# Kernel optimization log

Hardware: AMD Instinct MI355X
Metric: run time of the kernel (lower is better)

The kernel has to match this reference:

```python
import jax, jax.numpy as jnp
import numpy as np
from jax import lax

B, IMG = 2, 512
FMC, HID, A, NC = 1024, 512, 9, 21
RED, POOL, TOP, IOU_THR = 16, 7, 20, 0.3
NEG = -1e30
# 3 scales x 3 aspect ratios (w, h)
ANCHOR_WH = np.array([[s * np.sqrt(r), s / np.sqrt(r)] for s in (64.0, 128.0, 256.0) for r in (0.5, 1.0, 2.0)], dtype=np.float32)


def conv(x, w, b, stride, pad):
    y = lax.conv_general_dilated(x, w, (stride, stride), pad, dimension_numbers=('NCHW', 'OIHW', 'NCHW'))
    return y + b[None, :, None, None]


def make_anchors(H, W, stride):
    cy = (jnp.arange(H, dtype=jnp.float32) + 0.5) * stride
    cx = (jnp.arange(W, dtype=jnp.float32) + 0.5) * stride
    cyg, cxg = jnp.meshgrid(cy, cx, indexing='ij')  # [H,W]
    wh = jnp.asarray(ANCHOR_WH)  # [A,2]
    w2 = wh[None, None, :, 0] / 2
    h2 = wh[None, None, :, 1] / 2
    cxg = cxg[:, :, None]
    cyg = cyg[:, :, None]
    boxes = jnp.stack([cxg - w2, cyg - h2, cxg + w2, cyg + h2], axis=-1)  # [H,W,A,4]
    return boxes.reshape(-1, 4)


def box_iou(b, boxes):
    # b [4], boxes [N,4], (x1,y1,x2,y2)
    ix1 = jnp.maximum(b[0], boxes[:, 0])
    iy1 = jnp.maximum(b[1], boxes[:, 1])
    ix2 = jnp.minimum(b[2], boxes[:, 2])
    iy2 = jnp.minimum(b[3], boxes[:, 3])
    inter = jnp.maximum(ix2 - ix1, 0.0) * jnp.maximum(iy2 - iy1, 0.0)
    ab = jnp.maximum(b[2] - b[0], 0.0) * jnp.maximum(b[3] - b[1], 0.0)
    ar = jnp.maximum(boxes[:, 2] - boxes[:, 0], 0.0) * jnp.maximum(boxes[:, 3] - boxes[:, 1], 0.0)
    return inter / (ab + ar - inter + 1e-8)


def nms_one(boxes, scores):
    # greedy NMS, fixed TOP selections
    n = scores.shape[0]
    idxs = jnp.arange(n)

    def step(s, _):
        i = jnp.argmax(s)
        b, sc = boxes[i], s[i]
        s = jnp.where((box_iou(b, boxes) > IOU_THR) | (idxs == i), NEG, s)
        return s, (b, sc)

    _, (bs, ss) = lax.scan(step, scores, None, length=TOP)
    return bs, ss  # [TOP,4], [TOP]


def roi_align_one(fm_b, boxes):
    # fm_b [C,H,W], boxes [R,4] in image coords -> [R,C,POOL,POOL]
    C, H, W = fm_b.shape
    b = boxes / RED
    t = (jnp.arange(POOL, dtype=jnp.float32) + 0.5) / POOL
    xs = b[:, 0:1] + jnp.maximum(b[:, 2] - b[:, 0], 0.0)[:, None] * t[None]  # [R,P]
    ys = b[:, 1:2] + jnp.maximum(b[:, 3] - b[:, 1], 0.0)[:, None] * t[None]
    x = jnp.clip(xs[:, None, :], 0.0, W - 1.0) * jnp.ones((1, POOL, 1), jnp.float32)  # [R,P,P]
    y = jnp.clip(ys[:, :, None], 0.0, H - 1.0) * jnp.ones((1, 1, POOL), jnp.float32)
    x0f, y0f = jnp.floor(x), jnp.floor(y)
    x0, y0 = x0f.astype(jnp.int32), y0f.astype(jnp.int32)
    x1 = jnp.minimum(x0 + 1, W - 1)
    y1 = jnp.minimum(y0 + 1, H - 1)
    lx, ly = x - x0f, y - y0f
    v00 = fm_b[:, y0, x0]
    v01 = fm_b[:, y0, x1]
    v10 = fm_b[:, y1, x0]
    v11 = fm_b[:, y1, x1]  # [C,R,P,P]
    out = v00 * (1 - ly) * (1 - lx) + v01 * (1 - ly) * lx + v10 * ly * (1 - lx) + v11 * ly * lx
    return out.transpose(1, 0, 2, 3)


def setup_inputs() -> dict:
    key = jax.random.key(0)
    ks = jax.random.split(key, 16)
    s = 0.02
    return {
        'img': jax.random.normal(ks[0], (B, 3, IMG, IMG), jnp.float32),
        'img_id': jnp.arange(B, dtype=jnp.int32),
        'cnn_w': jax.random.normal(ks[1], (FMC, 3, RED, RED), jnp.float32) * s,
        'cnn_b': jnp.zeros((FMC,), jnp.float32),
        'rpn_w': jax.random.normal(ks[2], (HID, FMC, 3, 3), jnp.float32) * s,
        'rpn_b': jnp.zeros((HID,), jnp.float32),
        'rpn_reg_w': jax.random.normal(ks[3], (A * 4, HID, 1, 1), jnp.float32) * s,
        'rpn_reg_b': jnp.zeros((A * 4,), jnp.float32),
        'rpn_cls_w': jax.random.normal(ks[4], (A, HID, 1, 1), jnp.float32) * s,
        'rpn_cls_b': jnp.zeros((A,), jnp.float32),
        'fc_w': jax.random.normal(ks[5], (FMC * POOL * POOL, 1024), jnp.float32) * 0.005,
        'fc_b': jnp.zeros((1024,), jnp.float32),
        'reg_w': jax.random.normal(ks[6], (1024, 4), jnp.float32) * s,
        'reg_b': jnp.zeros((4,), jnp.float32),
        'cls_w': jax.random.normal(ks[7], (1024, NC), jnp.float32) * s,
        'cls_b': jnp.zeros((NC,), jnp.float32),
    }


def reference(img, img_id, cnn_w, cnn_b, rpn_w, rpn_b, rpn_reg_w, rpn_reg_b, rpn_cls_w, rpn_cls_b, fc_w, fc_b, reg_w, reg_b, cls_w, cls_b):
    fm = jax.nn.relu(conv(img, cnn_w, cnn_b, RED, 'VALID'))  # [B,1024,32,32]
    Bn, C, H, W = fm.shape
    # sliding-window(3x3, stride 1) + per-slice RPN == 3x3 SAME conv + 1x1 heads
    h = jax.nn.relu(conv(fm, rpn_w, rpn_b, 1, 'SAME'))
    rpn_reg = conv(h, rpn_reg_w, rpn_reg_b, 1, 'SAME').transpose(0, 2, 3, 1).reshape(Bn, -1, 4)  # (h,w,a) order
    rpn_cls = conv(h, rpn_cls_w, rpn_cls_b, 1, 'SAME').transpose(0, 2, 3, 1).reshape(Bn, -1)
    anchors = make_anchors(H, W, RED)  # [H*W*A,4]
    nms_reg, nms_cls = jax.vmap(nms_one)(rpn_reg + anchors[None], rpn_cls)  # [B,TOP,4],[B,TOP]
    pooled = jax.vmap(roi_align_one)(fm[img_id], nms_reg)  # [B,TOP,C,P,P]
    flat = pooled.reshape(Bn * TOP, -1)
    hf = jax.nn.relu(flat @ fc_w + fc_b)
    rcnn_reg = (hf @ reg_w + reg_b).reshape(Bn, -1, 4)
    rcnn_cls = (hf @ cls_w + cls_b).reshape(Bn, TOP, -1)
    return rpn_reg, rpn_cls, nms_reg, nms_cls, rcnn_reg, rcnn_cls, anchors
```

## Files before the change

kernel.cpp:

```cpp
#include <hip/hip_runtime.h>
#include <math.h>


#define NEGV (-1e30f)

typedef unsigned short u16;
typedef float v4f __attribute__((ext_vector_type(4)));
typedef short short8 __attribute__((ext_vector_type(8)));

#define O_RPN_REG 0
#define O_RPN_CLS 73728
#define O_NMS_REG 92160
#define O_NMS_CLS 92320
#define O_RCNN_REG 92360
#define O_RCNN_CLS 92520
#define O_ANCH 93360

#define W_FM   0u
#define W_ZERO 2097152u
#define W_PROP 3145728u
#define W_SCR  3219456u
#define W_FLAT 3237888u
#define W_HF   5244928u
#define W_A1H  5285888u
#define W_A1L  6072320u
#define W_B1H  6858752u
#define W_B1L  7251968u
#define W_FMH  7645184u
#define W_FML  8693760u
#define W_B2H  9742336u
#define W_B2L  12101632u
#define W_PART 14460928u

static __device__ __forceinline__ float relu_(float v) { return fmaxf(v, 0.0f); }

static __device__ __forceinline__ void gload16(const void* g, void* l) {
    __builtin_amdgcn_global_load_lds(
        (const __attribute__((address_space(1))) unsigned int*)g,
        (__attribute__((address_space(3))) unsigned int*)l, 16, 0, 0);
}

static __device__ __forceinline__ u16 bf16_rtne(float x) {
    unsigned int u = __float_as_uint(x);
    unsigned int r = u + 0x7fffu + ((u >> 16) & 1u);
    return (u16)(r >> 16);
}
static __device__ __forceinline__ void split2(float x, u16& h, u16& l) {
    h = bf16_rtne(x);
    const float hf = __uint_as_float(((unsigned int)h) << 16);
    l = bf16_rtne(x - hf);
}
static __device__ __forceinline__ void split8_store(const float* v, u16* dsth, u16* dstl) {
    uint4 H, Lo;
    u16 h0, l0, h1, l1;
    split2(v[0], h0, l0); split2(v[1], h1, l1);
    H.x = (unsigned)h0 | ((unsigned)h1 << 16); Lo.x = (unsigned)l0 | ((unsigned)l1 << 16);
    split2(v[2], h0, l0); split2(v[3], h1, l1);
    H.y = (unsigned)h0 | ((unsigned)h1 << 16); Lo.y = (unsigned)l0 | ((unsigned)l1 << 16);
    split2(v[4], h0, l0); split2(v[5], h1, l1);
    H.z = (unsigned)h0 | ((unsigned)h1 << 16); Lo.z = (unsigned)l0 | ((unsigned)l1 << 16);
    split2(v[6], h0, l0); split2(v[7], h1, l1);
    H.w = (unsigned)h0 | ((unsigned)h1 << 16); Lo.w = (unsigned)l0 | ((unsigned)l1 << 16);
    *(uint4*)dsth = H; *(uint4*)dstl = Lo;
}

static __device__ __forceinline__ void anchor_wh(int a, float& w2, float& h2) {
    double s = (a < 3) ? 64.0 : (a < 6) ? 128.0 : 256.0;
    int rm = a - (a / 3) * 3;
    double r = (rm == 0) ? 0.5 : (rm == 1) ? 1.0 : 2.0;
    double sq = sqrt(r);
    w2 = (float)(s * sq) * 0.5f;
    h2 = (float)(s / sq) * 0.5f;
}

__global__ __launch_bounds__(256) void k_prep_all(
        const float* __restrict__ img, u16* __restrict__ a1h, u16* __restrict__ a1l,
        float* __restrict__ zbuf,
        const float* __restrict__ cnnw, u16* __restrict__ b1h, u16* __restrict__ b1l,
        const float* __restrict__ rpnw, u16* __restrict__ b2h, u16* __restrict__ b2l) {
    __shared__ __align__(16) u16 sh[9216];
    __shared__ __align__(16) u16 sl[9216];
    const int bx = blockIdx.x, tid = threadIdx.x;
    if (bx < 1536) {
        if (bx == 0 && tid < 64) zbuf[tid] = 0.0f;
        const int idx = bx * 256 + tid;
        const int m = idx / 192, kq = (idx - m * 192) * 4;
        const int b = m >> 10, i = (m >> 5) & 31, j = m & 31;
        const int c = kq >> 8, rem = kq & 255, y = rem >> 4, x = rem & 15;
        const float4 v = *(const float4*)(img + ((size_t)((b * 3 + c) * 512 + i * 16 + y)) * 512 + j * 16 + x);
        ushort4 H, Lo;
        split2(v.x, H.x, Lo.x); split2(v.y, H.y, Lo.y);
        split2(v.z, H.z, Lo.z); split2(v.w, H.w, Lo.w);
        *(ushort4*)(a1h + (size_t)idx * 4) = H;
        *(ushort4*)(a1l + (size_t)idx * 4) = Lo;
    } else if (bx < 2304) {
        const int idx = (bx - 1536) * 256 + tid;
        const float4 v = *(const float4*)(cnnw + (size_t)idx * 4);
        ushort4 H, Lo;
        split2(v.x, H.x, Lo.x); split2(v.y, H.y, Lo.y);
        split2(v.z, H.z, Lo.z); split2(v.w, H.w, Lo.w);
        *(ushort4*)(b1h + (size_t)idx * 4) = H;
        *(ushort4*)(b1l + (size_t)idx * 4) = Lo;
    } else {
        const int oc = bx - 2304;
        const float* p = rpnw + (size_t)oc * 9216;
        for (int i = tid * 4; i < 9216; i += 1024) {
            const float4 v = *(const float4*)(p + i);
            ushort4 H, Lo;
            split2(v.x, H.x, Lo.x); split2(v.y, H.y, Lo.y);
            split2(v.z, H.z, Lo.z); split2(v.w, H.w, Lo.w);
            *(ushort4*)(sh + i) = H;
            *(ushort4*)(sl + i) = Lo;
        }
        __syncthreads();
        const int ic4 = tid * 4;
#pragma unroll
        for (int d = 0; d < 9; ++d) {
            ushort4 H, Lo;
            H.x = sh[(ic4 + 0) * 9 + d]; Lo.x = sl[(ic4 + 0) * 9 + d];
            H.y = sh[(ic4 + 1) * 9 + d]; Lo.y = sl[(ic4 + 1) * 9 + d];
            H.z = sh[(ic4 + 2) * 9 + d]; Lo.z = sl[(ic4 + 2) * 9 + d];
            H.w = sh[(ic4 + 3) * 9 + d]; Lo.w = sl[(ic4 + 3) * 9 + d];
            const size_t o = (size_t)oc * 9216 + d * 1024 + ic4;
            *(ushort4*)(b2h + o) = H;
            *(ushort4*)(b2l + o) = Lo;
        }
    }
}

template<int MODE>
__global__ __launch_bounds__(256, 3) void k_gemm(
        const u16* __restrict__ Agh, const u16* __restrict__ Agl,
        const u16* __restrict__ Bgh, const u16* __restrict__ Bgl,
        const float* __restrict__ bias, float* __restrict__ Cout, float* __restrict__ Cout2,
        const int KA, const int KB, const int nchunk, const int ldc, const int do_bias_relu,
        u16* __restrict__ outH, u16* __restrict__ outL, const float* __restrict__ zbuf) {
    __shared__ __align__(16) u16 AsH[2 * 128 * 32];
    __shared__ __align__(16) u16 AsL[2 * 128 * 32];
    __shared__ __align__(16) u16 BsH[2 * 64 * 32];
    __shared__ __align__(16) u16 BsL[2 * 64 * 32];
    const int tid = threadIdx.x;
    const int w = tid >> 6, L = tid & 63;
    const int q = L >> 4, lr = L & 15;
    const int wm = w >> 1, wn = w & 1;
    const int m0 = blockIdx.x * 128, n0 = blockIdx.y * 64;
    const int zbase = blockIdx.z * nchunk;
    float* C;
    if (MODE == 1) {
        C = (blockIdx.z < 4) ? (Cout + (size_t)blockIdx.z * (2048u * 512u))
                             : (Cout2 + (size_t)(blockIdx.z - 4) * (2048u * 512u));
    } else {
        C = (blockIdx.z == 0) ? Cout : Cout2;
    }
    const int seg = L & 3, rsub = L >> 2;

    u16* lseg[6];
    int lsz[6];
    const u16* gbase[6];
    int arow_b[6], arow_i[6], arow_j[6];
    int kindv[6];
#pragma unroll
    for (int s = 0; s < 6; ++s) {
        const int idx = w * 6 + s;
        int kind, inst;
        if (idx < 8)       { kind = 0; inst = idx; }
        else if (idx < 16) { kind = 1; inst = idx - 8; }
        else if (idx < 20) { kind = 2; inst = idx - 16; }
        else               { kind = 3; inst = idx - 20; }
        kindv[s] = kind;
        const int r = inst * 16 + rsub;
        u16* lb = (kind == 0) ? AsH : (kind == 1) ? AsL : (kind == 2) ? BsH : BsL;
        lseg[s] = lb + r * 32 + seg * 8;
        lsz[s] = (kind < 2) ? (128 * 32) : (64 * 32);
        arow_b[s] = 0; arow_i[s] = 0; arow_j[s] = 0;
        if (kind >= 2) {
            const u16* gb = (kind == 2) ? Bgh : Bgl;
            gbase[s] = gb + (size_t)(n0 + r) * KB + seg * 8;
        } else if (MODE == 0) {
            const u16* gb = (kind == 0) ? Agh : Agl;
            gbase[s] = gb + (size_t)(m0 + r) * KA + seg * 8;
        } else {
            const int m = m0 + r;
            arow_b[s] = m >> 10; arow_i[s] = (m >> 5) & 31; arow_j[s] = m & 31;
            gbase[s] = (kind == 0) ? Agh : Agl;
        }
    }

    v4f acc[4][2];
#pragma unroll
    for (int t = 0; t < 4; ++t)
#pragma unroll
        for (int u2 = 0; u2 < 2; ++u2) acc[t][u2] = (v4f){0.f, 0.f, 0.f, 0.f};

#define ISSUE(c_, bb_) do { \
    int d_, ic_, kB_; \
    if (MODE == 0) { const int g_ = zbase + (c_); kB_ = g_ * 32; d_ = 0; ic_ = kB_; } \
    else { const int g_ = zbase + (c_); d_ = g_ >> 5; ic_ = (g_ & 31) << 5; kB_ = d_ * 1024 + ic_; } \
    const int di_ = d_ / 3, dj_ = d_ - di_ * 3; \
    _Pragma("unroll") \
    for (int s = 0; s < 6; ++s) { \
        const u16* gsrc_; \
        if (kindv[s] >= 2) gsrc_ = gbase[s] + kB_; \
        else if (MODE == 0) gsrc_ = gbase[s] + ic_; \
        else { \
            const int y_ = arow_i[s] + di_ - 1, x_ = arow_j[s] + dj_ - 1; \
            const bool ok_ = ((unsigned)y_ < 32u) && ((unsigned)x_ < 32u); \
            const int yc_ = ok_ ? y_ : 0, xc_ = ok_ ? x_ : 0; \
            const u16* ga_ = gbase[s] + (size_t)((arow_b[s] * 32 + yc_) * 32 + xc_) * 1024 + ic_ + seg * 8; \
            gsrc_ = ok_ ? ga_ : (const u16*)zbuf; \
        } \
        gload16(gsrc_, lseg[s] + (bb_) * lsz[s]); \
    } \
} while (0)

    int cur = 0;
    ISSUE(0, 0);
    for (int c = 0; c < nchunk; ++c) {
        __syncthreads();
        if (c + 1 < nchunk) ISSUE(c + 1, cur ^ 1);
        const int ao = cur * (128 * 32), bo = cur * (64 * 32);
        short8 ah[4], al[4], bh[2], bl[2];
#pragma unroll
        for (int t = 0; t < 4; ++t) {
            ah[t] = *(const short8*)(AsH + ao + (wm * 64 + t * 16 + lr) * 32 + q * 8);
            al[t] = *(const short8*)(AsL + ao + (wm * 64 + t * 16 + lr) * 32 + q * 8);
        }
#pragma unroll
        for (int u2 = 0; u2 < 2; ++u2) {
            bh[u2] = *(const short8*)(BsH + bo + (wn * 32 + u2 * 16 + lr) * 32 + q * 8);
            bl[u2] = *(const short8*)(BsL + bo + (wn * 32 + u2 * 16 + lr) * 32 + q * 8);
        }
#pragma unroll
        for (int t = 0; t < 4; ++t)
#pragma unroll
            for (int u2 = 0; u2 < 2; ++u2) {
                acc[t][u2] = __builtin_amdgcn_mfma_f32_16x16x32_bf16(ah[t], bh[u2], acc[t][u2], 0, 0, 0);
                acc[t][u2] = __builtin_amdgcn_mfma_f32_16x16x32_bf16(ah[t], bl[u2], acc[t][u2], 0, 0, 0);
                acc[t][u2] = __builtin_amdgcn_mfma_f32_16x16x32_bf16(al[t], bh[u2], acc[t][u2], 0, 0, 0);
            }
        cur ^= 1;
    }
#undef ISSUE

#pragma unroll
    for (int t = 0; t < 4; ++t) {
        const int row = m0 + wm * 64 + t * 16 + q * 4;
#pragma unroll
        for (int u2 = 0; u2 < 2; ++u2) {
            const int col = n0 + wn * 32 + u2 * 16 + lr;
            const float bv = do_bias_relu ? bias[col] : 0.f;
#pragma unroll
            for (int r = 0; r < 4; ++r) {
                float vv = acc[t][u2][r];
                if (do_bias_relu) vv = relu_(vv + bv);
                C[(size_t)(row + r) * ldc + col] = vv;
                if (MODE == 0 && outH != nullptr) {
                    u16 hh, ll; split2(vv, hh, ll);
                    outH[(size_t)(row + r) * 1024 + col] = hh;
                    outL[(size_t)(row + r) * 1024 + col] = ll;
                }
            }
        }
    }
}

__global__ void k_c1_reduce(const float* __restrict__ p1, const float* __restrict__ cb,
                            float* __restrict__ fm, u16* __restrict__ fmh, u16* __restrict__ fml) {
    const size_t o = ((size_t)blockIdx.x * 256 + threadIdx.x) * 4;
    float4 a = *(const float4*)(fm + o);
    const float4 b4 = *(const float4*)(p1 + o);
    const float4 bb = *(const float4*)(cb + (o & 1023));
    a.x = relu_(a.x + b4.x + bb.x);
    a.y = relu_(a.y + b4.y + bb.y);
    a.z = relu_(a.z + b4.z + bb.z);
    a.w = relu_(a.w + b4.w + bb.w);
    *(float4*)(fm + o) = a;
    ushort4 H, Lo;
    split2(a.x, H.x, Lo.x); split2(a.y, H.y, Lo.y);
    split2(a.z, H.z, Lo.z); split2(a.w, H.w, Lo.w);
    *(ushort4*)(fmh + o) = H;
    *(ushort4*)(fml + o) = Lo;
}

__global__ __launch_bounds__(256) void k_rpn_heads2(const float* __restrict__ partA,
        const float* __restrict__ partB,
        const float* __restrict__ rpnb,
        const float* __restrict__ regw, const float* __restrict__ regb,
        const float* __restrict__ clsw, const float* __restrict__ clsb,
        float* __restrict__ out, float* __restrict__ prop, float* __restrict__ scr) {
    __shared__ __align__(16) float hrow[8][512];
    const int tid = threadIdx.x;
    const int m0 = blockIdx.x * 8;
#pragma unroll
    for (int i = 0; i < 4; ++i) {
        const int f = i * 256 + tid;
        const int r = f >> 7, c4 = (f & 127) * 4;
        const size_t ro = (size_t)(m0 + r) * 512 + c4;
        const float4 a0 = *(const float4*)(partA + ro);
        const float4 a1 = *(const float4*)(partA + 1048576u + ro);
        const float4 a2 = *(const float4*)(partA + 2097152u + ro);
        const float4 a3 = *(const float4*)(partA + 3145728u + ro);
        const float4 a4 = *(const float4*)(partB + ro);
        const float4 a5 = *(const float4*)(partB + 1048576u + ro);
        const float4 bb = *(const float4*)(rpnb + c4);
        float4 o;
        o.x = relu_(a0.x + a1.x + a2.x + a3.x + a4.x + a5.x + bb.x);
        o.y = relu_(a0.y + a1.y + a2.y + a3.y + a4.y + a5.y + bb.y);
        o.z = relu_(a0.z + a1.z + a2.z + a3.z + a4.z + a5.z + bb.z);
        o.w = relu_(a0.w + a1.w + a2.w + a3.w + a4.w + a5.w + bb.w);
        *(float4*)&hrow[r][c4] = o;
    }
    __syncthreads();
    const int w = tid >> 6, lane = tid & 63;
#pragma unroll
    for (int rr = 0; rr < 2; ++rr) {
        const int lrow = w * 2 + rr;
        const int m = m0 + lrow;
        const int b = m >> 10, qd = m & 1023, ii = qd >> 5, jj = qd & 31;
        const float cx = ((float)jj + 0.5f) * 16.f, cy = ((float)ii + 0.5f) * 16.f;
        if (lane < 45) {
            const int isreg = (lane < 36);
            const float* wp = isreg ? (regw + (size_t)lane * 512) : (clsw + (size_t)(lane - 36) * 512);
            float acc2 = isreg ? regb[lane] : clsb[lane - 36];
            const float* hr = hrow[lrow];
            for (int k = 0; k < 512; k += 4) {
                const float4 wv = *(const float4*)(wp + k);
                acc2 += hr[k + 0] * wv.x; acc2 += hr[k + 1] * wv.y;
                acc2 += hr[k + 2] * wv.z; acc2 += hr[k + 3] * wv.w;
            }
            if (isreg) {
                out[O_RPN_REG + (size_t)b * 36864 + qd * 36 + lane] = acc2;
                const int a = lane >> 2, cc = lane & 3;
                float w2, h2; anchor_wh(a, w2, h2);
                const float av = (cc == 0) ? cx - w2 : (cc == 1) ? cy - h2 : (cc == 2) ? cx + w2 : cy + h2;
                prop[(size_t)b * 36864 + qd * 36 + lane] = acc2 + av;
            } else {
                const int n = lane - 36;
                out[O_RPN_CLS + (size_t)b * 9216 + qd * 9 + n] = acc2;
                scr[(size_t)b * 9216 + qd * 9 + n] = acc2;
            }
        } else if (b == 0 && lane < 54) {
            const int a = lane - 45;
            float w2, h2; anchor_wh(a, w2, h2);
            const float4 av4 = make_float4(cx - w2, cy - h2, cx + w2, cy + h2);
            *(float4*)(out + O_ANCH + (size_t)(qd * 9 + a) * 4) = av4;
        }
    }
}

__global__ __launch_bounds__(512) void k_nms3(const float* __restrict__ prop,
        const float* __restrict__ scr, float* __restrict__ out) {
    __shared__ float wv_[2][8];
    __shared__ int wi_[2][8];
    const int b = blockIdx.x, tid = threadIdx.x;
    const int lane = tid & 63, wid = tid >> 6;
    const float* P = prop + (size_t)b * 36864;
    float4 bx[18]; float sv[18];
#pragma unroll
    for (int k = 0; k < 18; ++k) {
        const int i = tid * 18 + k;
        bx[k] = *(const float4*)(P + (size_t)i * 4);
        sv[k] = scr[b * 9216 + i];
    }
    for (int t = 0; t < 20; ++t) {
        float bv = -3.4e38f; int bi = 0;
#pragma unroll
        for (int k = 0; k < 18; ++k)
            if (sv[k] > bv) { bv = sv[k]; bi = tid * 18 + k; }
#pragma unroll
        for (int off = 1; off < 64; off <<= 1) {
            const float ov = __shfl_xor(bv, off);
            const int oi = __shfl_xor(bi, off);
            if (ov > bv || (ov == bv && oi < bi)) { bv = ov; bi = oi; }
        }
        if (lane == 0) { wv_[t & 1][wid] = bv; wi_[t & 1][wid] = bi; }
        __syncthreads();
        float rb = wv_[t & 1][0]; int sel = wi_[t & 1][0];
#pragma unroll
        for (int j = 1; j < 8; ++j) {
            const float v2 = wv_[t & 1][j]; const int i2 = wi_[t & 1][j];
            if (v2 > rb || (v2 == rb && i2 < sel)) { rb = v2; sel = i2; }
        }
        const float4 bb = *(const float4*)(P + (size_t)sel * 4);
        if (tid == 0) {
            *(float4*)(out + O_NMS_REG + (size_t)(b * 20 + t) * 4) = bb;
            out[O_NMS_CLS + b * 20 + t] = rb;
        }
        const float ab2 = fmaxf(bb.z - bb.x, 0.f) * fmaxf(bb.w - bb.y, 0.f);
#pragma unroll
        for (int k = 0; k < 18; ++k) {
            const float ix1 = fmaxf(bb.x, bx[k].x), iy1 = fmaxf(bb.y, bx[k].y);
            const float ix2 = fminf(bb.z, bx[k].z), iy2 = fminf(bb.w, bx[k].w);
            const float inter = fmaxf(ix2 - ix1, 0.f) * fmaxf(iy2 - iy1, 0.f);
            const float ar2 = fmaxf(bx[k].z - bx[k].x, 0.f) * fmaxf(bx[k].w - bx[k].y, 0.f);
            const float iou = inter / (ab2 + ar2 - inter + 1e-8f);
            if (iou > 0.3f || (tid * 18 + k) == sel) sv[k] = NEGV;
        }
    }
}

__global__ __launch_bounds__(256) void k_roi(const float* __restrict__ fm,
        const int* __restrict__ img_id, const float* __restrict__ nreg,
        float* __restrict__ flat, const float* __restrict__ fcb, float* __restrict__ hf) {
    __shared__ float tile[12544];
    const int hid = (((blockIdx.z * 20 + blockIdx.y) * 4) + blockIdx.x) * 256 + threadIdx.x;
    hf[hid] = fcb[hid & 1023];
    const int c0 = blockIdx.x * 256;
    const int roi = blockIdx.y, b = blockIdx.z;
    const float* bx = nreg + (size_t)(b * 20 + roi) * 4;
    const float b0 = bx[0] * 0.0625f, b1 = bx[1] * 0.0625f;
    const float b2 = bx[2] * 0.0625f, b3 = bx[3] * 0.0625f;
    const float wd = fmaxf(b2 - b0, 0.f), hg = fmaxf(b3 - b1, 0.f);
    const int bb = img_id[b];
    const float* fmb = fm + (size_t)bb * (32 * 32 * 1024);
    const int c = c0 + threadIdx.x;
    for (int py = 0; py < 7; ++py) {
        const float tyv = ((float)py + 0.5f) / 7.0f;
        const float ycv = fminf(fmaxf(b1 + hg * tyv, 0.f), 31.f);
        const float y0f = floorf(ycv);
        const int y0 = (int)y0f, y1 = min(y0 + 1, 31);
        const float ly = ycv - y0f, omly = 1.f - ly;
        for (int px = 0; px < 7; ++px) {
            const float txv = ((float)px + 0.5f) / 7.0f;
            const float xcv = fminf(fmaxf(b0 + wd * txv, 0.f), 31.f);
            const float x0f = floorf(xcv);
            const int x0 = (int)x0f, x1 = min(x0 + 1, 31);
            const float lx = xcv - x0f, omlx = 1.f - lx;
            const int o00 = ((y0 * 32) + x0) << 10, o01 = ((y0 * 32) + x1) << 10;
            const int o10 = ((y1 * 32) + x0) << 10, o11 = ((y1 * 32) + x1) << 10;
            const float v00 = fmb[o00 + c], v01 = fmb[o01 + c];
            const float v10 = fmb[o10 + c], v11 = fmb[o11 + c];
            tile[threadIdx.x * 49 + py * 7 + px] =
                ((v00 * omly) * omlx) + ((v01 * omly) * lx)
                + ((v10 * ly) * omlx) + ((v11 * ly) * lx);
        }
    }
    __syncthreads();
    const size_t ob = (size_t)(b * 20 + roi) * 50176 + (size_t)c0 * 49;
    for (int i = threadIdx.x * 4; i < 12544; i += 1024)
        *(float4*)(flat + ob + i) = *(const float4*)&tile[i];
}

__global__ __launch_bounds__(256, 2) void k_fc_mfma(const float* __restrict__ flat,
        const float* __restrict__ fcw, float* __restrict__ hf) {
    __shared__ __align__(16) u16 AsH[4 * 48 * 8];
    __shared__ __align__(16) u16 AsL[4 * 48 * 8];
    __shared__ __align__(16) u16 BsH[4 * 128 * 8];
    __shared__ __align__(16) u16 BsL[4 * 128 * 8];
    const int tid = threadIdx.x;
    const int w = tid >> 6, L = tid & 63, q = L >> 4, lr = L & 15;
    const int n0 = blockIdx.x * 128, kb = blockIdx.y * 512;
    if (tid < 32) {
        const int oct = tid >> 3, m = 40 + (tid & 7);
        *(uint4*)(AsH + (oct * 48 + m) * 8) = make_uint4(0, 0, 0, 0);
        *(uint4*)(AsL + (oct * 48 + m) * 8) = make_uint4(0, 0, 0, 0);
    }
    const int am = tid >> 2, aoct = tid & 3;
    const float* abase = flat + (size_t)am * 50176 + kb + aoct * 8;
    const int bcolI = tid & 127, bkh = tid >> 7;
    const float* bcol = fcw + n0 + bcolI;

    v4f acc[3][2];
#pragma unroll
    for (int mt = 0; mt < 3; ++mt)
#pragma unroll
        for (int nt = 0; nt < 2; ++nt) acc[mt][nt] = (v4f){0.f, 0.f, 0.f, 0.f};

    float areg[8];
    float breg[2][8];

#define LOADF(c_) do { \
    if (tid < 160) { \
        const float4 u_ = *(const float4*)(abase + (c_) * 32); \
        const float4 v_ = *(const float4*)(abase + (c_) * 32 + 4); \
        areg[0] = u_.x; areg[1] = u_.y; areg[2] = u_.z; areg[3] = u_.w; \
        areg[4] = v_.x; areg[5] = v_.y; areg[6] = v_.z; areg[7] = v_.w; \
    } \
    _Pragma("unroll") \
    for (int o_ = 0; o_ < 2; ++o_) \
        _Pragma("unroll") \
        for (int j_ = 0; j_ < 8; ++j_) \
            breg[o_][j_] = bcol[(size_t)(kb + (c_) * 32 + bkh * 16 + o_ * 8 + j_) * 1024]; \
} while (0)

    LOADF(0);
    for (int c = 0; c < 16; ++c) {
        __syncthreads();
        if (tid < 160)
            split8_store(areg, AsH + (aoct * 48 + am) * 8, AsL + (aoct * 48 + am) * 8);
#pragma unroll
        for (int o = 0; o < 2; ++o)
            split8_store(breg[o], BsH + ((bkh * 2 + o) * 128 + bcolI) * 8,
                                  BsL + ((bkh * 2 + o) * 128 + bcolI) * 8);
        __syncthreads();
        if (c + 1 < 16) LOADF(c + 1);
        short8 ah[3], al[3], bh2[2], bl2[2];
#pragma unroll
        for (int mt = 0; mt < 3; ++mt) {
            ah[mt] = *(const short8*)(AsH + (q * 48 + mt * 16 + lr) * 8);
            al[mt] = *(const short8*)(AsL + (q * 48 + mt * 16 + lr) * 8);
        }
#pragma unroll
        for (int nt = 0; nt < 2; ++nt) {
            bh2[nt] = *(const short8*)(BsH + (q * 128 + w * 32 + nt * 16 + lr) * 8);
            bl2[nt] = *(const short8*)(BsL + (q * 128 + w * 32 + nt * 16 + lr) * 8);
        }
#pragma unroll
        for (int mt = 0; mt < 3; ++mt)
#pragma unroll
            for (int nt = 0; nt < 2; ++nt) {
                acc[mt][nt] = __builtin_amdgcn_mfma_f32_16x16x32_bf16(ah[mt], bh2[nt], acc[mt][nt], 0, 0, 0);
                acc[mt][nt] = __builtin_amdgcn_mfma_f32_16x16x32_bf16(ah[mt], bl2[nt], acc[mt][nt], 0, 0, 0);
                acc[mt][nt] = __builtin_amdgcn_mfma_f32_16x16x32_bf16(al[mt], bh2[nt], acc[mt][nt], 0, 0, 0);
            }
    }
#undef LOADF

#pragma unroll
    for (int mt = 0; mt < 3; ++mt) {
#pragma unroll
        for (int nt = 0; nt < 2; ++nt) {
#pragma unroll
            for (int r = 0; r < 4; ++r) {
                const int row = mt * 16 + q * 4 + r;
                if (row < 40)
                    atomicAdd(hf + (size_t)row * 1024 + n0 + w * 32 + nt * 16 + lr, acc[mt][nt][r]);
            }
        }
    }
}

__global__ __launch_bounds__(64) void k_heads(const float* __restrict__ hf,
        const float* __restrict__ regw, const float* __restrict__ regb,
        const float* __restrict__ clsw, const float* __restrict__ clsb,
        float* __restrict__ out) {
    __shared__ __align__(16) float hrow[1024];
    const int m = blockIdx.x, tid = threadIdx.x;
    for (int i = tid * 4; i < 1024; i += 256) {
        const float4 v = *(const float4*)(hf + (size_t)m * 1024 + i);
        hrow[i + 0] = relu_(v.x); hrow[i + 1] = relu_(v.y);
        hrow[i + 2] = relu_(v.z); hrow[i + 3] = relu_(v.w);
    }
    __syncthreads();
    if (tid < 25) {
        float acc2 = 0.f;
        if (tid < 4) {
            for (int k = 0; k < 1024; ++k) acc2 += hrow[k] * regw[(size_t)k * 4 + tid];
            out[O_RCNN_REG + m * 4 + tid] = acc2 + regb[tid];
        } else {
            const int n = tid - 4;
            for (int k = 0; k < 1024; ++k) acc2 += hrow[k] * clsw[(size_t)k * 21 + n];
            out[O_RCNN_CLS + m * 21 + n] = acc2 + clsb[n];
        }
    }
}

extern "C" void kernel_launch(void* const* d_in, const int* in_sizes, int n_in,
                              void* d_out, int out_size, void* d_ws, size_t ws_size,
                              hipStream_t stream) {
    (void)in_sizes; (void)n_in; (void)out_size; (void)ws_size;
    const float* img       = (const float*)d_in[0];
    const int*   img_id    = (const int*)  d_in[1];
    const float* cnn_w     = (const float*)d_in[2];
    const float* cnn_b     = (const float*)d_in[3];
    const float* rpn_w     = (const float*)d_in[4];
    const float* rpn_b     = (const float*)d_in[5];
    const float* rpn_reg_w = (const float*)d_in[6];
    const float* rpn_reg_b = (const float*)d_in[7];
    const float* rpn_cls_w = (const float*)d_in[8];
    const float* rpn_cls_b = (const float*)d_in[9];
    const float* fc_w      = (const float*)d_in[10];
    const float* fc_b      = (const float*)d_in[11];
    const float* reg_w     = (const float*)d_in[12];
    const float* reg_b     = (const float*)d_in[13];
    const float* cls_w     = (const float*)d_in[14];
    const float* cls_b     = (const float*)d_in[15];
    float* out = (float*)d_out;
    float* ws  = (float*)d_ws;

    float* fm   = ws + W_FM;
    float* zbuf = ws + W_ZERO;
    float* prop = ws + W_PROP;
    float* scr  = ws + W_SCR;
    float* flat = ws + W_FLAT;
    float* hf   = ws + W_HF;
    u16* a1h = (u16*)(ws + W_A1H);
    u16* a1l = (u16*)(ws + W_A1L);
    u16* b1h = (u16*)(ws + W_B1H);
    u16* b1l = (u16*)(ws + W_B1L);
    u16* fmh = (u16*)(ws + W_FMH);
    u16* fml = (u16*)(ws + W_FML);
    u16* b2h = (u16*)(ws + W_B2H);
    u16* b2l = (u16*)(ws + W_B2L);
    float* partA = ws + W_FLAT;
    float* partB = ws + W_PART;

    k_prep_all<<<2816, 256, 0, stream>>>(img, a1h, a1l, zbuf, cnn_w, b1h, b1l, rpn_w, b2h, b2l);
    k_gemm<0><<<dim3(16, 16, 2), 256, 0, stream>>>(a1h, a1l, b1h, b1l, cnn_b, fm, partB,
                                                   768, 768, 12, 1024, 0, nullptr, nullptr, zbuf);
    k_c1_reduce<<<2048, 256, 0, stream>>>(partB, cnn_b, fm, fmh, fml);
    k_gemm<1><<<dim3(16, 8, 6), 256, 0, stream>>>(fmh, fml, b2h, b2l, nullptr, partA, partB,
                                                  1024, 9216, 48, 512, 0, nullptr, nullptr, zbuf);
    k_rpn_heads2<<<256, 256, 0, stream>>>(partA, partB, rpn_b, rpn_reg_w, rpn_reg_b, rpn_cls_w, rpn_cls_b,
                                          out, prop, scr);
    k_nms3<<<2, 512, 0, stream>>>(prop, scr, out);
    k_roi<<<dim3(4, 20, 2), 256, 0, stream>>>(fm, img_id, out + O_NMS_REG, flat, fc_b, hf);
    k_fc_mfma<<<dim3(8, 98), 256, 0, stream>>>(flat, fc_w, hf);
    k_heads<<<40, 64, 0, stream>>>(hf, reg_w, reg_b, cls_w, cls_b, out);
}
```

Before: 605.4 us.

## Use 128x128 GEMM tiles with atomic split-K accumulation into bias-initialized outputs

The split-bf16 MFMA GEMM tile grows from 128x64 to 128x128, giving each warp a 4x4 accumulator block so more MFMAs share each LDS fragment load. Split-K partial buffers and their multi-way reduction are replaced by float atomicAdd into output buffers that are pre-filled with bias, in k_prep_all for the backbone conv and in k_c1_reduce for the RPN conv. The RPN conv split changes from 6 to 8 K-slices, and the heads kernel now reads a single accumulated buffer. The cost is heavy atomic traffic, a non-deterministic summation order, and more registers per thread (occupancy hint lowered from 3 to 2).

```diff
diff --git a/kernel.cpp b/kernel.cpp
--- a/kernel.cpp
+++ b/kernel.cpp
@@ -77,7 +77,8 @@
         const float* __restrict__ img, u16* __restrict__ a1h, u16* __restrict__ a1l,
         float* __restrict__ zbuf,
         const float* __restrict__ cnnw, u16* __restrict__ b1h, u16* __restrict__ b1l,
-        const float* __restrict__ rpnw, u16* __restrict__ b2h, u16* __restrict__ b2l) {
+        const float* __restrict__ rpnw, u16* __restrict__ b2h, u16* __restrict__ b2l,
+        const float* __restrict__ cnnb, float* __restrict__ fm) {
     __shared__ __align__(16) u16 sh[9216];
     __shared__ __align__(16) u16 sl[9216];
     const int bx = blockIdx.x, tid = threadIdx.x;
@@ -101,7 +102,7 @@
         split2(v.z, H.z, Lo.z); split2(v.w, H.w, Lo.w);
         *(ushort4*)(b1h + (size_t)idx * 4) = H;
         *(ushort4*)(b1l + (size_t)idx * 4) = Lo;
-    } else {
+    } else if (bx < 2816) {
         const int oc = bx - 2304;
         const float* p = rpnw + (size_t)oc * 9216;
         for (int i = tid * 4; i < 9216; i += 1024) {
@@ -125,91 +126,82 @@
             *(ushort4*)(b2h + o) = H;
             *(ushort4*)(b2l + o) = Lo;
         }
+    } else {
+        const size_t o = ((size_t)(bx - 2816) * 256 + tid) * 4;
+        *(float4*)(fm + o) = *(const float4*)(cnnb + (o & 1023));
     }
 }
 
 template<int MODE>
-__global__ __launch_bounds__(256, 3) void k_gemm(
+__global__ __launch_bounds__(256, 2) void k_gemm(
         const u16* __restrict__ Agh, const u16* __restrict__ Agl,
         const u16* __restrict__ Bgh, const u16* __restrict__ Bgl,
-        const float* __restrict__ bias, float* __restrict__ Cout, float* __restrict__ Cout2,
-        const int KA, const int KB, const int nchunk, const int ldc, const int do_bias_relu,
-        u16* __restrict__ outH, u16* __restrict__ outL, const float* __restrict__ zbuf) {
+        float* __restrict__ Cacc,
+        const int KA, const int KB, const int nchunk, const int ldc,
+        const float* __restrict__ zbuf) {
     __shared__ __align__(16) u16 AsH[2 * 128 * 32];
     __shared__ __align__(16) u16 AsL[2 * 128 * 32];
-    __shared__ __align__(16) u16 BsH[2 * 64 * 32];
-    __shared__ __align__(16) u16 BsL[2 * 64 * 32];
+    __shared__ __align__(16) u16 BsH[2 * 128 * 32];
+    __shared__ __align__(16) u16 BsL[2 * 128 * 32];
     const int tid = threadIdx.x;
     const int w = tid >> 6, L = tid & 63;
     const int q = L >> 4, lr = L & 15;
     const int wm = w >> 1, wn = w & 1;
-    const int m0 = blockIdx.x * 128, n0 = blockIdx.y * 64;
+    const int m0 = blockIdx.x * 128, n0 = blockIdx.y * 128;
     const int zbase = blockIdx.z * nchunk;
-    float* C;
-    if (MODE == 1) {
-        C = (blockIdx.z < 4) ? (Cout + (size_t)blockIdx.z * (2048u * 512u))
-                             : (Cout2 + (size_t)(blockIdx.z - 4) * (2048u * 512u));
-    } else {
-        C = (blockIdx.z == 0) ? Cout : Cout2;
-    }
-    const int seg = L & 3, rsub = L >> 2;
-
-    u16* lseg[6];
-    int lsz[6];
-    const u16* gbase[6];
-    int arow_b[6], arow_i[6], arow_j[6];
-    int kindv[6];
-#pragma unroll
-    for (int s = 0; s < 6; ++s) {
-        const int idx = w * 6 + s;
-        int kind, inst;
-        if (idx < 8)       { kind = 0; inst = idx; }
-        else if (idx < 16) { kind = 1; inst = idx - 8; }
-        else if (idx < 20) { kind = 2; inst = idx - 16; }
-        else               { kind = 3; inst = idx - 20; }
-        kindv[s] = kind;
-        const int r = inst * 16 + rsub;
-        u16* lb = (kind == 0) ? AsH : (kind == 1) ? AsL : (kind == 2) ? BsH : BsL;
-        lseg[s] = lb + r * 32 + seg * 8;
-        lsz[s] = (kind < 2) ? (128 * 32) : (64 * 32);
-        arow_b[s] = 0; arow_i[s] = 0; arow_j[s] = 0;
-        if (kind >= 2) {
-            const u16* gb = (kind == 2) ? Bgh : Bgl;
-            gbase[s] = gb + (size_t)(n0 + r) * KB + seg * 8;
+    const int rr = tid >> 2, seg = tid & 3;
+
+    u16* lbase[8];
+    const u16* gb[8];
+    long aoff[2]; int ai[2], aj[2];
+#pragma unroll
+    for (int s = 0; s < 8; ++s) {
+        const int buf = s >> 1, half = s & 1;
+        const int r = half * 64 + rr;
+        u16* lb = (buf == 0) ? AsH : (buf == 1) ? AsL : (buf == 2) ? BsH : BsL;
+        lbase[s] = lb + (half * 256 + tid) * 8;
+        if (buf >= 2) {
+            const u16* g0 = (buf == 2) ? Bgh : Bgl;
+            gb[s] = g0 + (size_t)(n0 + r) * KB + seg * 8;
         } else if (MODE == 0) {
-            const u16* gb = (kind == 0) ? Agh : Agl;
-            gbase[s] = gb + (size_t)(m0 + r) * KA + seg * 8;
+            const u16* g0 = (buf == 0) ? Agh : Agl;
+            gb[s] = g0 + (size_t)(m0 + r) * KA + seg * 8;
         } else {
             const int m = m0 + r;
-            arow_b[s] = m >> 10; arow_i[s] = (m >> 5) & 31; arow_j[s] = m & 31;
-            gbase[s] = (kind == 0) ? Agh : Agl;
-        }
-    }
-
-    v4f acc[4][2];
+            const int b_ = m >> 10, i_ = (m >> 5) & 31, j_ = m & 31;
+            if (buf == 0) { aoff[half] = (long)b_ * 1048576 + seg * 8; ai[half] = i_; aj[half] = j_; }
+            gb[s] = (buf == 0) ? Agh : Agl;
+        }
+    }
+
+    v4f acc[4][4];
 #pragma unroll
     for (int t = 0; t < 4; ++t)
 #pragma unroll
-        for (int u2 = 0; u2 < 2; ++u2) acc[t][u2] = (v4f){0.f, 0.f, 0.f, 0.f};
+        for (int u = 0; u < 4; ++u) acc[t][u] = (v4f){0.f, 0.f, 0.f, 0.f};
 
 #define ISSUE(c_, bb_) do { \
-    int d_, ic_, kB_; \
-    if (MODE == 0) { const int g_ = zbase + (c_); kB_ = g_ * 32; d_ = 0; ic_ = kB_; } \
-    else { const int g_ = zbase + (c_); d_ = g_ >> 5; ic_ = (g_ & 31) << 5; kB_ = d_ * 1024 + ic_; } \
+    const int g_ = zbase + (c_); \
+    int d_ = 0, ic_ = 0; \
+    if (MODE == 1) { d_ = g_ >> 5; ic_ = (g_ & 31) << 5; } \
+    const int kOff_ = (MODE == 0) ? g_ * 32 : (d_ * 1024 + ic_); \
     const int di_ = d_ / 3, dj_ = d_ - di_ * 3; \
+    long goffA_[2]; bool okA_[2]; \
+    if (MODE == 1) { \
+        _Pragma("unroll") \
+        for (int h_ = 0; h_ < 2; ++h_) { \
+            const int y_ = ai[h_] + di_ - 1, x_ = aj[h_] + dj_ - 1; \
+            okA_[h_] = ((unsigned)y_ < 32u) && ((unsigned)x_ < 32u); \
+            goffA_[h_] = aoff[h_] + (long)(okA_[h_] ? y_ : 0) * 32768 \
+                       + (long)(okA_[h_] ? x_ : 0) * 1024 + ic_; \
+        } \
+    } \
     _Pragma("unroll") \
-    for (int s = 0; s < 6; ++s) { \
+    for (int s = 0; s < 8; ++s) { \
         const u16* gsrc_; \
-        if (kindv[s] >= 2) gsrc_ = gbase[s] + kB_; \
-        else if (MODE == 0) gsrc_ = gbase[s] + ic_; \
-        else { \
-            const int y_ = arow_i[s] + di_ - 1, x_ = arow_j[s] + dj_ - 1; \
-            const bool ok_ = ((unsigned)y_ < 32u) && ((unsigned)x_ < 32u); \
-            const int yc_ = ok_ ? y_ : 0, xc_ = ok_ ? x_ : 0; \
-            const u16* ga_ = gbase[s] + (size_t)((arow_b[s] * 32 + yc_) * 32 + xc_) * 1024 + ic_ + seg * 8; \
-            gsrc_ = ok_ ? ga_ : (const u16*)zbuf; \
-        } \
-        gload16(gsrc_, lseg[s] + (bb_) * lsz[s]); \
+        if (MODE == 0 || s >= 4) gsrc_ = gb[s] + kOff_; \
+        else gsrc_ = okA_[s & 1] ? (gb[s] + goffA_[s & 1]) : (const u16*)zbuf; \
+        gload16(gsrc_, lbase[s] + (bb_) * 4096); \
     } \
 } while (0)
 
@@ -218,25 +210,25 @@
     for (int c = 0; c < nchunk; ++c) {
         __syncthreads();
         if (c + 1 < nchunk) ISSUE(c + 1, cur ^ 1);
-        const int ao = cur * (128 * 32), bo = cur * (64 * 32);
-        short8 ah[4], al[4], bh[2], bl[2];
+        const int ao = cur * 4096;
+        short8 ah[4], al[4], bh[4], bl[4];
 #pragma unroll
         for (int t = 0; t < 4; ++t) {
             ah[t] = *(const short8*)(AsH + ao + (wm * 64 + t * 16 + lr) * 32 + q * 8);
             al[t] = *(const short8*)(AsL + ao + (wm * 64 + t * 16 + lr) * 32 + q * 8);
         }
 #pragma unroll
-        for (int u2 = 0; u2 < 2; ++u2) {
-            bh[u2] = *(const short8*)(BsH + bo + (wn * 32 + u2 * 16 + lr) * 32 + q * 8);
-            bl[u2] = *(const short8*)(BsL + bo + (wn * 32 + u2 * 16 + lr) * 32 + q * 8);
+        for (int u = 0; u < 4; ++u) {
+            bh[u] = *(const short8*)(BsH + ao + (wn * 64 + u * 16 + lr) * 32 + q * 8);
+            bl[u] = *(const short8*)(BsL + ao + (wn * 64 + u * 16 + lr) * 32 + q * 8);
         }
 #pragma unroll
         for (int t = 0; t < 4; ++t)
 #pragma unroll
-            for (int u2 = 0; u2 < 2; ++u2) {
-                acc[t][u2] = __builtin_amdgcn_mfma_f32_16x16x32_bf16(ah[t], bh[u2], acc[t][u2], 0, 0, 0);
-                acc[t][u2] = __builtin_amdgcn_mfma_f32_16x16x32_bf16(ah[t], bl[u2], acc[t][u2], 0, 0, 0);
-                acc[t][u2] = __builtin_amdgcn_mfma_f32_16x16x32_bf16(al[t], bh[u2], acc[t][u2], 0, 0, 0);
+            for (int u = 0; u < 4; ++u) {
+                acc[t][u] = __builtin_amdgcn_mfma_f32_16x16x32_bf16(ah[t], bh[u], acc[t][u], 0, 0, 0);
+                acc[t][u] = __builtin_amdgcn_mfma_f32_16x16x32_bf16(ah[t], bl[u], acc[t][u], 0, 0, 0);
+                acc[t][u] = __builtin_amdgcn_mfma_f32_16x16x32_bf16(al[t], bh[u], acc[t][u], 0, 0, 0);
             }
         cur ^= 1;
     }
@@ -246,45 +238,34 @@
     for (int t = 0; t < 4; ++t) {
         const int row = m0 + wm * 64 + t * 16 + q * 4;
 #pragma unroll
-        for (int u2 = 0; u2 < 2; ++u2) {
-            const int col = n0 + wn * 32 + u2 * 16 + lr;
-            const float bv = do_bias_relu ? bias[col] : 0.f;
-#pragma unroll
-            for (int r = 0; r < 4; ++r) {
-                float vv = acc[t][u2][r];
-                if (do_bias_relu) vv = relu_(vv + bv);
-                C[(size_t)(row + r) * ldc + col] = vv;
-                if (MODE == 0 && outH != nullptr) {
-                    u16 hh, ll; split2(vv, hh, ll);
-                    outH[(size_t)(row + r) * 1024 + col] = hh;
-                    outL[(size_t)(row + r) * 1024 + col] = ll;
-                }
-            }
-        }
-    }
-}
-
-__global__ void k_c1_reduce(const float* __restrict__ p1, const float* __restrict__ cb,
+        for (int u = 0; u < 4; ++u) {
+            const int col = n0 + wn * 64 + u * 16 + lr;
+#pragma unroll
+            for (int r = 0; r < 4; ++r)
+                atomicAdd(Cacc + (size_t)(row + r) * ldc + col, acc[t][u][r]);
+        }
+    }
+}
+
+__global__ void k_c1_reduce(const float* __restrict__ rpnb, float* __restrict__ partB,
                             float* __restrict__ fm, u16* __restrict__ fmh, u16* __restrict__ fml) {
-    const size_t o = ((size_t)blockIdx.x * 256 + threadIdx.x) * 4;
+    const int gid = blockIdx.x * 256 + threadIdx.x;
+    const size_t o = (size_t)gid * 4;
     float4 a = *(const float4*)(fm + o);
-    const float4 b4 = *(const float4*)(p1 + o);
-    const float4 bb = *(const float4*)(cb + (o & 1023));
-    a.x = relu_(a.x + b4.x + bb.x);
-    a.y = relu_(a.y + b4.y + bb.y);
-    a.z = relu_(a.z + b4.z + bb.z);
-    a.w = relu_(a.w + b4.w + bb.w);
+    a.x = relu_(a.x); a.y = relu_(a.y); a.z = relu_(a.z); a.w = relu_(a.w);
     *(float4*)(fm + o) = a;
     ushort4 H, Lo;
     split2(a.x, H.x, Lo.x); split2(a.y, H.y, Lo.y);
     split2(a.z, H.z, Lo.z); split2(a.w, H.w, Lo.w);
     *(ushort4*)(fmh + o) = H;
     *(ushort4*)(fml + o) = Lo;
-}
-
-__global__ __launch_bounds__(256) void k_rpn_heads2(const float* __restrict__ partA,
-        const float* __restrict__ partB,
-        const float* __restrict__ rpnb,
+    if (gid < 262144) {
+        const int c = (gid * 4) & 511;
+        *(float4*)(partB + (size_t)gid * 4) = *(const float4*)(rpnb + c);
+    }
+}
+
+__global__ __launch_bounds__(256) void k_rpn_heads2(const float* __restrict__ partB,
         const float* __restrict__ regw, const float* __restrict__ regb,
         const float* __restrict__ clsw, const float* __restrict__ clsb,
         float* __restrict__ out, float* __restrict__ prop, float* __restrict__ scr) {
@@ -295,19 +276,9 @@
     for (int i = 0; i < 4; ++i) {
         const int f = i * 256 + tid;
         const int r = f >> 7, c4 = (f & 127) * 4;
-        const size_t ro = (size_t)(m0 + r) * 512 + c4;
-        const float4 a0 = *(const float4*)(partA + ro);
-        const float4 a1 = *(const float4*)(partA + 1048576u + ro);
-        const float4 a2 = *(const float4*)(partA + 2097152u + ro);
-        const float4 a3 = *(const float4*)(partA + 3145728u + ro);
-        const float4 a4 = *(const float4*)(partB + ro);
-        const float4 a5 = *(const float4*)(partB + 1048576u + ro);
-        const float4 bb = *(const float4*)(rpnb + c4);
+        const float4 p = *(const float4*)(partB + (size_t)(m0 + r) * 512 + c4);
         float4 o;
-        o.x = relu_(a0.x + a1.x + a2.x + a3.x + a4.x + a5.x + bb.x);
-        o.y = relu_(a0.y + a1.y + a2.y + a3.y + a4.y + a5.y + bb.y);
-        o.z = relu_(a0.z + a1.z + a2.z + a3.z + a4.z + a5.z + bb.z);
-        o.w = relu_(a0.w + a1.w + a2.w + a3.w + a4.w + a5.w + bb.w);
+        o.x = relu_(p.x); o.y = relu_(p.y); o.z = relu_(p.z); o.w = relu_(p.w);
         *(float4*)&hrow[r][c4] = o;
     }
     __syncthreads();
@@ -592,16 +563,16 @@
     u16* fml = (u16*)(ws + W_FML);
     u16* b2h = (u16*)(ws + W_B2H);
     u16* b2l = (u16*)(ws + W_B2L);
-    float* partA = ws + W_FLAT;
     float* partB = ws + W_PART;
 
-    k_prep_all<<<2816, 256, 0, stream>>>(img, a1h, a1l, zbuf, cnn_w, b1h, b1l, rpn_w, b2h, b2l);
-    k_gemm<0><<<dim3(16, 16, 2), 256, 0, stream>>>(a1h, a1l, b1h, b1l, cnn_b, fm, partB,
-                                                   768, 768, 12, 1024, 0, nullptr, nullptr, zbuf);
-    k_c1_reduce<<<2048, 256, 0, stream>>>(partB, cnn_b, fm, fmh, fml);
-    k_gemm<1><<<dim3(16, 8, 6), 256, 0, stream>>>(fmh, fml, b2h, b2l, nullptr, partA, partB,
-                                                  1024, 9216, 48, 512, 0, nullptr, nullptr, zbuf);
-    k_rpn_heads2<<<256, 256, 0, stream>>>(partA, partB, rpn_b, rpn_reg_w, rpn_reg_b, rpn_cls_w, rpn_cls_b,
+    k_prep_all<<<4864, 256, 0, stream>>>(img, a1h, a1l, zbuf, cnn_w, b1h, b1l,
+                                         rpn_w, b2h, b2l, cnn_b, fm);
+    k_gemm<0><<<dim3(16, 8, 4), 256, 0, stream>>>(a1h, a1l, b1h, b1l, fm,
+                                                  768, 768, 6, 1024, zbuf);
+    k_c1_reduce<<<2048, 256, 0, stream>>>(rpn_b, partB, fm, fmh, fml);
+    k_gemm<1><<<dim3(16, 4, 8), 256, 0, stream>>>(fmh, fml, b2h, b2l, partB,
+                                                  1024, 9216, 36, 512, zbuf);
+    k_rpn_heads2<<<256, 256, 0, stream>>>(partB, rpn_reg_w, rpn_reg_b, rpn_cls_w, rpn_cls_b,
                                           out, prop, scr);
     k_nms3<<<2, 512, 0, stream>>>(prop, scr, out);
     k_roi<<<dim3(4, 20, 2), 256, 0, stream>>>(fm, img_id, out + O_NMS_REG, flat, fc_b, hf);
```

New measurement: 621.0 us. 1.03x slower.
